# Optimization experiments

Measured on AMD Instinct MI355X. Metric: run time of the kernel, lower is better.

The kernel has to match this reference:

```python
import jax, jax.numpy as jnp
import numpy as np

EPS = 1e-08
NUM_EMBEDDINGS = 8192
EMBEDDING_DIM = 256
N_TOKENS = 32768


def setup_inputs() -> dict:
    key = jax.random.key(0)
    k1, k2, k3 = jax.random.split(key, 3)
    input_data = jax.random.normal(k1, (N_TOKENS, EMBEDDING_DIM), dtype=jnp.float32)
    rand = jax.random.normal(k2, (N_TOKENS, EMBEDDING_DIM), dtype=jnp.float32)
    codebooks = jax.random.normal(k3, (NUM_EMBEDDINGS, EMBEDDING_DIM), dtype=jnp.float32)
    return {"input_data": input_data, "rand": rand, "codebooks": codebooks}


def reference(input_data, rand, codebooks):
    # d2: (N, K) -- this full matrix is what a fused kernel would avoid.
    d2 = (jnp.sum(input_data * input_data, axis=1, keepdims=True)
          - 2.0 * input_data @ codebooks.T
          + jnp.sum(codebooks * codebooks, axis=1)[None, :])
    min_idx = jnp.argmin(d2, axis=1)                      # (N,)
    hard_q = codebooks[min_idx]                           # (N, D)

    # Noise substitution: scale unit-ish gaussian noise to the residual norm.
    r_norm = jnp.linalg.norm(input_data - hard_q, axis=1, keepdims=True)
    n_norm = jnp.linalg.norm(rand, axis=1, keepdims=True)
    quantized_input = input_data + (r_norm / (n_norm + EPS)) * rand

    # Perplexity from codebook usage counts (no grad path in original).
    counts = jnp.zeros((NUM_EMBEDDINGS,), dtype=jnp.float32).at[min_idx].add(1.0)
    total = jnp.maximum(counts.sum(), 1.0)
    avg_probs = counts / total
    perplexity = jnp.exp(-jnp.sum(avg_probs * jnp.log(avg_probs + EPS)))
    num_unique_indices = jnp.sum(counts > 0).astype(jnp.int32)
    return quantized_input, perplexity, num_unique_indices
```

## Files before the change

kernel.cpp:

```cpp
#include <hip/hip_runtime.h>
#include <stdint.h>

#define N_TOKENS 32768
#define N_CODES  8192
#define DIM      256
#define EPSF     1e-8f

typedef __bf16 bf16x8 __attribute__((ext_vector_type(8)));
typedef float  f32x4  __attribute__((ext_vector_type(4)));

#define WS_CNORM_OFF  (4u*1024u*1024u)
#define WS_HIST_OFF   (WS_CNORM_OFF + N_CODES*4u)

__global__ __launch_bounds__(256) void k_prep(const float* __restrict__ cbf,
                                              unsigned short* __restrict__ cbh,
                                              float* __restrict__ cnorm,
                                              int* __restrict__ hist) {
    const int tid = blockIdx.x * 256 + threadIdx.x;
    if (tid < N_CODES) hist[tid] = 0;

    const int w = threadIdx.x >> 6;
    const int lane = threadIdx.x & 63;
    const int row = blockIdx.x * 4 + w;

    const float4 v = ((const float4*)(cbf + (size_t)row * DIM))[lane];
    float sq = v.x * v.x + v.y * v.y + v.z * v.z + v.w * v.w;

    ushort4 u;
    u.x = __builtin_bit_cast(unsigned short, (__bf16)v.x);
    u.y = __builtin_bit_cast(unsigned short, (__bf16)v.y);
    u.z = __builtin_bit_cast(unsigned short, (__bf16)v.z);
    u.w = __builtin_bit_cast(unsigned short, (__bf16)v.w);
    ((ushort4*)(cbh + (size_t)row * DIM))[lane] = u;

    #pragma unroll
    for (int d = 1; d < 64; d <<= 1) sq += __shfl_xor(sq, d);
    if (lane == 0) cnorm[row] = sq;
}

__global__ __launch_bounds__(512, 2) void k_argmin(const float* __restrict__ X,
                                                   const float* __restrict__ R,
                                                   const unsigned short* __restrict__ cbh,
                                                   const float* __restrict__ cnorm,
                                                   float* __restrict__ out,
                                                   int* __restrict__ hist) {
    __shared__ __attribute__((aligned(16))) char smem[135680];
    float* redv  = (float*)(smem + 131072);
    int*   redi  = (int*)(smem + 133120);
    float* maxvS = (float*)(smem + 135168);

    const int tid  = threadIdx.x;
    const int w    = tid >> 6;
    const int lane = tid & 63;
    const int lr   = lane & 15;
    const int lq   = lane >> 4;
    const int th   = w >> 2;
    const int wc   = w & 3;
    const int r0   = blockIdx.x * 128;
    const int mycol = wc * 16 + lr;

    {
        const float4* Xf4 = (const float4*)(X + (size_t)(r0 + 16 * w) * DIM);
        #pragma unroll
        for (int i = 0; i < 16; ++i) {
            const float4 v = Xf4[i * 64 + lane];
            ushort4 u;
            u.x = __builtin_bit_cast(unsigned short, (__bf16)v.x);
            u.y = __builtin_bit_cast(unsigned short, (__bf16)v.y);
            u.z = __builtin_bit_cast(unsigned short, (__bf16)v.z);
            u.w = __builtin_bit_cast(unsigned short, (__bf16)v.w);
            *(ushort4*)(smem + (16 * w + i) * 544 + lane * 8) = u;
        }
    }
    __syncthreads();

    bf16x8 A[4][8];
    #pragma unroll
    for (int mf = 0; mf < 4; ++mf)
        #pragma unroll
        for (int kc = 0; kc < 8; ++kc)
            A[mf][kc] = *(const bf16x8*)(smem + (64 * th + mf * 16 + lr) * 544 + kc * 64 + lq * 16);
    __syncthreads();

    const int half = lane >> 5, l5 = lane & 31;
    int srcoff[8];
    #pragma unroll
    for (int d = 0; d < 8; ++d) {
        const int c = 16 * wc + 2 * d + half;
        const int j = (l5 - c) & 31;
        srcoff[d] = c * 512 + j * 16;
    }
    const char* cbb = (const char*)cbh;
    char* mybase = smem + w * 16384;

    #pragma unroll
    for (int d = 0; d < 8; ++d)
        __builtin_amdgcn_global_load_lds(
            (const __attribute__((address_space(1))) unsigned int*)(cbb + srcoff[d]),
            (__attribute__((address_space(3))) unsigned int*)(mybase + d * 1024),
            16, 0, 0);

    float maxv[16];
    int   maxi[16];
    #pragma unroll
    for (int i = 0; i < 16; ++i) { maxv[i] = -3.4e38f; maxi[i] = 0; }

    for (int cc = 0; cc < 128; ++cc) {
        const int cur = (cc & 1) * 8192;

        asm volatile("s_waitcnt vmcnt(0)" ::: "memory");

        if (cc + 1 < 128) {
            const char* src = cbb + (size_t)(cc + 1) * 32768;
            const int nxt = ((cc + 1) & 1) * 8192;
            #pragma unroll
            for (int d = 0; d < 8; ++d)
                __builtin_amdgcn_global_load_lds(
                    (const __attribute__((address_space(1))) unsigned int*)(src + srcoff[d]),
                    (__attribute__((address_space(3))) unsigned int*)(mybase + nxt + d * 1024),
                    16, 0, 0);
        }

        const float cn = cnorm[cc * 64 + mycol];

        bf16x8 b[8];
        #pragma unroll
        for (int kc = 0; kc < 8; ++kc)
            b[kc] = *(const bf16x8*)(mybase + cur + lr * 512 +
                                     (((kc * 4 + lq + mycol) & 31) << 4));

        f32x4 acc[4];
        #pragma unroll
        for (int mf = 0; mf < 4; ++mf) {
            acc[mf][0] = 0.f; acc[mf][1] = 0.f; acc[mf][2] = 0.f; acc[mf][3] = 0.f;
        }

        #pragma unroll
        for (int kc = 0; kc < 8; ++kc)
            #pragma unroll
            for (int mf = 0; mf < 4; ++mf)
                acc[mf] = __builtin_amdgcn_mfma_f32_16x16x32_bf16(A[mf][kc], b[kc], acc[mf], 0, 0, 0);

        const int col = cc * 64 + mycol;
        #pragma unroll
        for (int mf = 0; mf < 4; ++mf)
            #pragma unroll
            for (int r = 0; r < 4; ++r) {
                const float v = fmaf(-0.5f, cn, acc[mf][r]);
                const int j = mf * 4 + r;
                if (v > maxv[j]) { maxv[j] = v; maxi[j] = col; }
            }
    }

    #pragma unroll
    for (int mf = 0; mf < 4; ++mf)
        #pragma unroll
        for (int r = 0; r < 4; ++r) {
            float v = maxv[mf * 4 + r]; int ix = maxi[mf * 4 + r];
            #pragma unroll
            for (int d = 1; d <= 8; d <<= 1) {
                const float ov = __shfl_xor(v, d);
                const int   oi = __shfl_xor(ix, d);
                if (ov > v || (ov == v && oi < ix)) { v = ov; ix = oi; }
            }
            if (lr == 0) {
                const int row = mf * 16 + lq * 4 + r;
                redv[w * 64 + row] = v; redi[w * 64 + row] = ix;
            }
        }
    __syncthreads();

    if (tid < 128) {
        const int t = tid, tth = t >> 6, tl = t & 63;
        float v = redv[(4 * tth) * 64 + tl]; int ix = redi[(4 * tth) * 64 + tl];
        #pragma unroll
        for (int ww = 1; ww < 4; ++ww) {
            const float ov = redv[(4 * tth + ww) * 64 + tl];
            const int   oi = redi[(4 * tth + ww) * 64 + tl];
            if (ov > v || (ov == v && oi < ix)) { v = ov; ix = oi; }
        }
        maxvS[t] = v;
        atomicAdd(&hist[ix], 1);
    }
    __syncthreads();

    for (int i = 0; i < 16; ++i) {
        const int tl = 16 * w + i;
        const int tok = r0 + tl;
        const float4 x = ((const float4*)(X + (size_t)tok * DIM))[lane];
        const float4 r = ((const float4*)(R + (size_t)tok * DIM))[lane];

        float x2 = x.x * x.x + x.y * x.y + x.z * x.z + x.w * x.w;
        float n2 = r.x * r.x + r.y * r.y + r.z * r.z + r.w * r.w;
        #pragma unroll
        for (int d = 1; d < 64; d <<= 1) {
            x2 += __shfl_xor(x2, d);
            n2 += __shfl_xor(n2, d);
        }
        const float mv = maxvS[tl];
        const float d2 = fmaxf(fmaf(-2.f, mv, x2), 0.f);
        const float s = sqrtf(d2) / (sqrtf(n2) + EPSF);

        float4 o;
        o.x = fmaf(s, r.x, x.x);
        o.y = fmaf(s, r.y, x.y);
        o.z = fmaf(s, r.z, x.z);
        o.w = fmaf(s, r.w, x.w);
        ((float4*)(out + (size_t)tok * DIM))[lane] = o;
    }
}

__global__ __launch_bounds__(1024) void k_stats(const int* __restrict__ hist,
                                                float* __restrict__ outs) {
    float s = 0.f; int u = 0;
    for (int b = threadIdx.x; b < N_CODES; b += 1024) {
        const float c = (float)hist[b];
        if (c > 0.f) ++u;
        const float p = c * (1.f / (float)N_TOKENS);
        s += p * logf(p + EPSF);
    }
    #pragma unroll
    for (int d = 1; d < 64; d <<= 1) {
        s += __shfl_xor(s, d);
        u += __shfl_xor(u, d);
    }
    __shared__ float ss[16];
    __shared__ int   su[16];
    const int w = threadIdx.x >> 6, lane = threadIdx.x & 63;
    if (lane == 0) { ss[w] = s; su[w] = u; }
    __syncthreads();
    if (threadIdx.x == 0) {
        float st = 0.f; int ut = 0;
        #pragma unroll
        for (int i = 0; i < 16; ++i) { st += ss[i]; ut += su[i]; }
        outs[0] = expf(-st);
        outs[1] = (float)ut;
    }
}

extern "C" void kernel_launch(void* const* d_in, const int* in_sizes, int n_in,
                              void* d_out, int out_size, void* d_ws, size_t ws_size,
                              hipStream_t stream) {
    const float* X = (const float*)d_in[0];
    const float* R = (const float*)d_in[1];
    const float* C = (const float*)d_in[2];
    float* out = (float*)d_out;

    char* ws = (char*)d_ws;
    unsigned short* cbh = (unsigned short*)ws;
    float* cnorm = (float*)(ws + WS_CNORM_OFF);
    int*   hist  = (int*)(ws + WS_HIST_OFF);

    k_prep  <<<N_CODES / 4,    256, 0, stream>>>(C, cbh, cnorm, hist);
    k_argmin<<<N_TOKENS / 128, 512, 0, stream>>>(X, R, cbh, cnorm, out, hist);
    k_stats <<<1, 1024, 0, stream>>>(hist, out + (size_t)N_TOKENS * DIM);
}
```

Before: 261.0 us.

## Fuse stats into argmin via last-block counter and hide cnorm load latency

Removes the separate single-block stats kernel by having the last finishing argmin block, detected with a global atomic counter reset in the prep kernel, compute perplexity and unique count from the histogram. Also issues the per-tile codebook-norm load with inline asm before the next-tile async copies and waits with vmcnt(8) after the MFMAs, so the load overlaps compute. This saves one kernel launch and its tail, at the cost of a global atomic and fence per block plus fragile hand-written wait counts.

Result: slower. 272.9 us (+4.5%).

```diff
diff --git a/kernel.cpp b/kernel.cpp
--- a/kernel.cpp
+++ b/kernel.cpp
@@ -11,6 +11,8 @@
 
 #define WS_CNORM_OFF  (4u*1024u*1024u)
 #define WS_HIST_OFF   (WS_CNORM_OFF + N_CODES*4u)
+
+__device__ int g_ctr;
 
 __global__ __launch_bounds__(256) void k_prep(const float* __restrict__ cbf,
                                               unsigned short* __restrict__ cbh,
@@ -18,6 +20,7 @@
                                               int* __restrict__ hist) {
     const int tid = blockIdx.x * 256 + threadIdx.x;
     if (tid < N_CODES) hist[tid] = 0;
+    if (tid == 0) g_ctr = 0;
 
     const int w = threadIdx.x >> 6;
     const int lane = threadIdx.x & 63;
@@ -45,6 +48,7 @@
                                                    float* __restrict__ out,
                                                    int* __restrict__ hist) {
     __shared__ __attribute__((aligned(16))) char smem[135680];
+    __shared__ int amLast;
     float* redv  = (float*)(smem + 131072);
     int*   redi  = (int*)(smem + 133120);
     float* maxvS = (float*)(smem + 135168);
@@ -110,6 +114,11 @@
 
         asm volatile("s_waitcnt vmcnt(0)" ::: "memory");
 
+        float cn;
+        asm volatile("global_load_dword %0, %1, off"
+                     : "=v"(cn)
+                     : "v"(cnorm + cc * 64 + mycol));
+
         if (cc + 1 < 128) {
             const char* src = cbb + (size_t)(cc + 1) * 32768;
             const int nxt = ((cc + 1) & 1) * 8192;
@@ -121,8 +130,6 @@
                     16, 0, 0);
         }
 
-        const float cn = cnorm[cc * 64 + mycol];
-
         bf16x8 b[8];
         #pragma unroll
         for (int kc = 0; kc < 8; ++kc)
@@ -140,6 +147,12 @@
             #pragma unroll
             for (int mf = 0; mf < 4; ++mf)
                 acc[mf] = __builtin_amdgcn_mfma_f32_16x16x32_bf16(A[mf][kc], b[kc], acc[mf], 0, 0, 0);
+
+        if (cc + 1 < 128) {
+            asm volatile("s_waitcnt vmcnt(8)" : "+v"(cn));
+        } else {
+            asm volatile("s_waitcnt vmcnt(0)" : "+v"(cn));
+        }
 
         const int col = cc * 64 + mycol;
         #pragma unroll
@@ -208,33 +221,36 @@
         o.w = fmaf(s, r.w, x.w);
         ((float4*)(out + (size_t)tok * DIM))[lane] = o;
     }
-}
-
-__global__ __launch_bounds__(1024) void k_stats(const int* __restrict__ hist,
-                                                float* __restrict__ outs) {
-    float s = 0.f; int u = 0;
-    for (int b = threadIdx.x; b < N_CODES; b += 1024) {
-        const float c = (float)hist[b];
-        if (c > 0.f) ++u;
-        const float p = c * (1.f / (float)N_TOKENS);
-        s += p * logf(p + EPSF);
-    }
-    #pragma unroll
-    for (int d = 1; d < 64; d <<= 1) {
-        s += __shfl_xor(s, d);
-        u += __shfl_xor(u, d);
-    }
-    __shared__ float ss[16];
-    __shared__ int   su[16];
-    const int w = threadIdx.x >> 6, lane = threadIdx.x & 63;
-    if (lane == 0) { ss[w] = s; su[w] = u; }
-    __syncthreads();
-    if (threadIdx.x == 0) {
-        float st = 0.f; int ut = 0;
-        #pragma unroll
-        for (int i = 0; i < 16; ++i) { st += ss[i]; ut += su[i]; }
-        outs[0] = expf(-st);
-        outs[1] = (float)ut;
+
+    if (tid == 0) {
+        __threadfence();
+        amLast = (atomicAdd(&g_ctr, 1) == (int)gridDim.x - 1);
+    }
+    __syncthreads();
+    if (amLast) {
+        float s = 0.f; int u = 0;
+        for (int b = tid; b < N_CODES; b += 512) {
+            const int c = __hip_atomic_load(&hist[b], __ATOMIC_RELAXED,
+                                            __HIP_MEMORY_SCOPE_AGENT);
+            if (c > 0) ++u;
+            const float p = (float)c * (1.f / (float)N_TOKENS);
+            s += p * logf(p + EPSF);
+        }
+        #pragma unroll
+        for (int d = 1; d < 64; d <<= 1) {
+            s += __shfl_xor(s, d);
+            u += __shfl_xor(u, d);
+        }
+        if (lane == 0) { redv[w] = s; redi[w] = u; }
+        __syncthreads();
+        if (tid == 0) {
+            float st = 0.f; int ut = 0;
+            #pragma unroll
+            for (int i = 0; i < 8; ++i) { st += redv[i]; ut += redi[i]; }
+            float* outs = out + (size_t)N_TOKENS * DIM;
+            outs[0] = expf(-st);
+            outs[1] = (float)ut;
+        }
     }
 }
 
@@ -253,5 +269,4 @@
 
     k_prep  <<<N_CODES / 4,    256, 0, stream>>>(C, cbh, cnorm, hist);
     k_argmin<<<N_TOKENS / 128, 512, 0, stream>>>(X, R, cbh, cnorm, out, hist);
-    k_stats <<<1, 1024, 0, stream>>>(hist, out + (size_t)N_TOKENS * DIM);
 }
```
